# Optimization experiments

Hardware: AMD Instinct MI355X
Metric: run time of the kernel (lower is better)

## Reference

```python
import jax, jax.numpy as jnp
import numpy as np

B, S, H, FMAX, MAXSENT, NHEADS, FFN, SEP = 32, 2048, 768, 32, 64, 12, 3072, 102


def setup_inputs() -> dict:
    key = jax.random.key(0)
    ks = jax.random.split(key, 16)
    sc = 0.02
    ids = jax.random.randint(ks[0], (B, S), 1000, 30000)
    pos = jnp.arange(S)
    # SEP token every 32 positions -> 63 variable-span 'sentences' per row
    ids = jnp.where((pos[None, :] % 32 == 0) & (pos[None, :] > 0), SEP, ids)
    n = lambda k, shp: sc * jax.random.normal(k, shp, jnp.float32)
    return {
        "hidden1": jax.random.normal(ks[1], (B, S, H), jnp.float32),
        "fact_cls": jax.random.normal(ks[2], (B, FMAX, H), jnp.float32),
        "Wp": n(ks[3], (H, H)), "bp": jnp.zeros((H,), jnp.float32), "vp": n(ks[4], (H, 1)),
        "Wq": n(ks[5], (H, H)), "bq": jnp.zeros((H,), jnp.float32),
        "Wk": n(ks[6], (H, H)), "bk": jnp.zeros((H,), jnp.float32),
        "Wv": n(ks[7], (H, H)), "bv": jnp.zeros((H,), jnp.float32),
        "Wo": n(ks[8], (H, H)), "bo": jnp.zeros((H,), jnp.float32),
        "ln1g": jnp.ones((H,), jnp.float32), "ln1b": jnp.zeros((H,), jnp.float32),
        "Wf1": n(ks[9], (H, FFN)), "bf1": jnp.zeros((FFN,), jnp.float32),
        "Wf2": n(ks[10], (FFN, H)), "bf2": jnp.zeros((H,), jnp.float32),
        "ln2g": jnp.ones((H,), jnp.float32), "ln2b": jnp.zeros((H,), jnp.float32),
        "input_ids": ids,
        "facts_count": jax.random.randint(ks[11], (B,), 0, FMAX),
        "max_sent": MAXSENT,
        "sep_id": SEP,
    }


def _ln(x, g, b):
    mu = jnp.mean(x, axis=-1, keepdims=True)
    var = jnp.mean((x - mu) ** 2, axis=-1, keepdims=True)
    return (x - mu) * jax.lax.rsqrt(var + 1e-12) * g + b


def _forward(hidden1, fact_cls, Wp, bp, vp, Wq, bq, Wk, bk, Wv, bv, Wo, bo,
             ln1g, ln1b, Wf1, bf1, Wf2, bf2, ln2g, ln2b,
             input_ids, facts_count, max_sent, sep_id):
    B_, S_ = input_ids.shape
    H_ = hidden1.shape[-1]
    # ---- ragged sentence spans: tokens strictly between SEPs, starting at pos 1 ----
    is_sep = input_ids == sep_id                      # [B,S]
    n_sent = jnp.sum(is_sep, axis=-1)                 # [B]
    seg = jnp.cumsum(is_sep, axis=1) - is_sep         # exclusive cumsum: sentence id per token
    pos = jnp.arange(S_)
    valid = (pos[None, :] >= 1) & (~is_sep) & (seg < n_sent[:, None])
    nseg = B_ * max_sent
    seg_id = jnp.where(valid, jnp.arange(B_)[:, None] * max_sent + seg, nseg).reshape(-1)
    # ---- attention pooling per sentence (segment softmax) ----
    scores = jnp.squeeze(jnp.tanh(hidden1 @ Wp + bp) @ vp, -1).reshape(-1)  # [B*S]
    vflat = valid.reshape(-1)
    m = jax.ops.segment_max(scores, seg_id, num_segments=nseg + 1)
    e = jnp.where(vflat, jnp.exp(scores - m[seg_id]), 0.0)
    z = jax.ops.segment_sum(e, seg_id, num_segments=nseg + 1)
    z = jnp.where(z > 0, z, 1.0)
    w = e / z[seg_id]
    sent = jax.ops.segment_sum(w[:, None] * hidden1.reshape(-1, H_), seg_id,
                               num_segments=nseg + 1)[:nseg].reshape(B_, max_sent, H_)
    # zero-sentence rows fall back to CLS embedding in slot 0
    sent = sent.at[:, 0].set(jnp.where((n_sent == 0)[:, None], hidden1[:, 0], sent[:, 0]))
    n_eff = jnp.maximum(n_sent, 1)
    # ---- pack sentences then facts into dense zero-padded buffer ----
    FMAX_ = fact_cls.shape[1]
    L = max_sent + FMAX_
    bidx = jnp.arange(B_)[:, None]
    buf = jnp.zeros((B_, L + 1, H_), hidden1.dtype)  # extra trash column L
    spos = jnp.where(jnp.arange(max_sent)[None, :] < n_eff[:, None],
                     jnp.arange(max_sent)[None, :], L)
    buf = buf.at[bidx, spos].set(sent)
    fpos = jnp.where(jnp.arange(FMAX_)[None, :] < facts_count[:, None],
                     n_eff[:, None] + jnp.arange(FMAX_)[None, :], L)
    buf = buf.at[bidx, fpos].set(fact_cls)
    x = buf[:, :L]
    amask = (jnp.arange(L)[None, :] < (n_eff + facts_count)[:, None]).astype(x.dtype)
    # ---- tf2 encoder layer (BERT post-LN) on packed sequence ----
    nh = NHEADS
    dh = H_ // nh
    q = (x @ Wq + bq).reshape(B_, L, nh, dh)
    k = (x @ Wk + bk).reshape(B_, L, nh, dh)
    v = (x @ Wv + bv).reshape(B_, L, nh, dh)
    att = jnp.einsum('blhd,bmhd->bhlm', q, k) / np.sqrt(dh).astype(x.dtype)
    att = att + (1.0 - amask)[:, None, None, :] * jnp.asarray(-1e9, x.dtype)
    att = jax.nn.softmax(att, axis=-1)
    ctx = jnp.einsum('bhlm,bmhd->blhd', att, v).reshape(B_, L, H_)
    x = _ln(x + ctx @ Wo + bo, ln1g, ln1b)
    h = jax.nn.gelu(x @ Wf1 + bf1, approximate=False) @ Wf2 + bf2
    x = _ln(x + h, ln2g, ln2b)
    return x[:, 0, :]


def reference(hidden1, fact_cls, Wp, bp, vp, Wq, bq, Wk, bk, Wv, bv, Wo, bo,
              ln1g, ln1b, Wf1, bf1, Wf2, bf2, ln2g, ln2b,
              input_ids, facts_count, max_sent, sep_id):
    return _forward(hidden1, fact_cls, Wp, bp, vp, Wq, bq, Wk, bk, Wv, bv, Wo, bo,
                    ln1g, ln1b, Wf1, bf1, Wf2, bf2, ln2g, ln2b,
                    input_ids, facts_count, max_sent, sep_id)
```

## Files before the change

kernel.cpp:

```cpp
#include <hip/hip_runtime.h>
#include <math.h>

#define Bz   32
#define Sz   2048
#define Hz   768
#define FMAXz 32
#define MSz  64
#define NHz  12
#define DHz  64
#define Lz   96
#define FFNz 3072
#define NTOK (Bz*Sz)

typedef short bf16x8 __attribute__((ext_vector_type(8)));
typedef float f32x4 __attribute__((ext_vector_type(4)));

__device__ __forceinline__ unsigned short f2bf(float f) {
  unsigned u = __float_as_uint(f);
  unsigned r = (u + 0x7fffu + ((u >> 16) & 1u)) >> 16;
  return (unsigned short)r;
}

__device__ __forceinline__ float fast_tanh(float x) {
  float e = __expf(2.0f * x);
  return 1.0f - 2.0f / (e + 1.0f);
}

__device__ __forceinline__ void gload16(const void* gp, void* lp) {
  __builtin_amdgcn_global_load_lds(
      (const __attribute__((address_space(1))) unsigned int*)(unsigned long long)(uintptr_t)gp,
      (__attribute__((address_space(3))) unsigned int*)(unsigned int)(uintptr_t)lp,
      16, 0, 0);
}

__global__ __launch_bounds__(256) void k_seg(
    const int* __restrict__ ids, const int* __restrict__ sep_p,
    int* __restrict__ segid, int* __restrict__ seppos,
    int* __restrict__ nsent, int* __restrict__ neff)
{
  int b = blockIdx.x, tid = threadIdx.x;
  int sep = *sep_p;
  __shared__ int cnt[256];
  __shared__ int total_s;
  const int* row = &ids[b*Sz];
  int base = tid*8;
  int loc[8];
  int c = 0;
  #pragma unroll
  for (int i = 0; i < 8; i++) { loc[i] = row[base+i]; c += (loc[i]==sep) ? 1 : 0; }
  cnt[tid] = c;
  __syncthreads();
  if (tid == 0) {
    int run = 0;
    for (int t = 0; t < 256; t++) { int tmp = cnt[t]; cnt[t] = run; run += tmp; }
    total_s = run;
    nsent[b] = run;
    neff[b]  = run > 0 ? run : 1;
  }
  __syncthreads();
  int total = total_s;
  int seg = cnt[tid];
  #pragma unroll
  for (int i = 0; i < 8; i++) {
    int s = base + i;
    bool issep = (loc[i]==sep);
    if (issep && seg < MSz) seppos[b*MSz + seg] = s;
    bool valid = (s >= 1) && !issep && (seg < total);
    segid[b*Sz + s] = valid ? seg : -1;
    if (issep) seg++;
  }
}

__global__ __launch_bounds__(256) void k_cvt_bf16(
    const float* __restrict__ src, unsigned short* __restrict__ dst, int n4)
{
  int i = blockIdx.x*256 + threadIdx.x;
  if (i >= n4) return;
  float4 v = ((const float4*)src)[i];
  ushort4 o;
  o.x = f2bf(v.x); o.y = f2bf(v.y); o.z = f2bf(v.z); o.w = f2bf(v.w);
  ((ushort4*)dst)[i] = o;
}

__global__ __launch_bounds__(256) void k_tr_cvt(
    const float* __restrict__ src, unsigned short* __restrict__ dst,
    int rows, int cols)
{
  __shared__ float t[32][33];
  int c0 = blockIdx.x*32, r0 = blockIdx.y*32;
  int cx = threadIdx.x & 31, ry = threadIdx.x >> 5;
  #pragma unroll
  for (int p = 0; p < 4; p++)
    t[ry + p*8][cx] = src[(size_t)(r0 + ry + p*8)*cols + c0 + cx];
  __syncthreads();
  #pragma unroll
  for (int p = 0; p < 4; p++) {
    int i = ry + p*8;
    dst[(size_t)(c0 + i)*rows + r0 + cx] = f2bf(t[cx][i]);
  }
}

__global__ __launch_bounds__(256) void k_scores_mfma(
    const unsigned short* __restrict__ h1b, const unsigned short* __restrict__ wpT,
    const float* __restrict__ bp, const float* __restrict__ vp,
    float* __restrict__ scores)
{
  __shared__ unsigned short As[4096];
  __shared__ unsigned short Bs[4096];
  __shared__ float bps[128], vps[128];
  const int tid = threadIdx.x;
  const int wave = tid >> 6, lane = tid & 63;
  const int ml = lane & 15, kg = lane >> 4;
  const int j0 = blockIdx.x * 128;
  const size_t tok0 = (size_t)blockIdx.y * 128;
  if (tid < 128) { bps[tid] = bp[j0+tid]; vps[tid] = vp[j0+tid]; }
  f32x4 acc[2][8];
  #pragma unroll
  for (int rt = 0; rt < 2; rt++)
    #pragma unroll
    for (int ct = 0; ct < 8; ct++) acc[rt][ct] = (f32x4){0.f,0.f,0.f,0.f};
  for (int k0 = 0; k0 < Hz; k0 += 32) {
    __syncthreads();
    #pragma unroll
    for (int l = 0; l < 2; l++) {
      int slot = l*256 + tid;
      int m = slot & 127, kgs = slot >> 7;
      gload16(&h1b[(tok0 + m)*Hz + k0 + kgs*8], &As[slot*8]);
      gload16(&wpT[(size_t)(j0 + m)*Hz + k0 + kgs*8], &Bs[slot*8]);
    }
    __syncthreads();
    bf16x8 af0 = *(const bf16x8*)&As[(kg*128 + wave*32 + ml)*8];
    bf16x8 af1 = *(const bf16x8*)&As[(kg*128 + wave*32 + 16 + ml)*8];
    #pragma unroll
    for (int ct = 0; ct < 8; ct++) {
      bf16x8 bfr = *(const bf16x8*)&Bs[(kg*128 + ct*16 + ml)*8];
      acc[0][ct] = __builtin_amdgcn_mfma_f32_16x16x32_bf16(af0, bfr, acc[0][ct], 0, 0, 0);
      acc[1][ct] = __builtin_amdgcn_mfma_f32_16x16x32_bf16(af1, bfr, acc[1][ct], 0, 0, 0);
    }
  }
  float part[2][4] = {{0,0,0,0},{0,0,0,0}};
  #pragma unroll
  for (int ct = 0; ct < 8; ct++) {
    int cl = ct*16 + ml;
    float bpv = bps[cl], vpv = vps[cl];
    #pragma unroll
    for (int rt = 0; rt < 2; rt++)
      #pragma unroll
      for (int i = 0; i < 4; i++)
        part[rt][i] += fast_tanh(acc[rt][ct][i] + bpv) * vpv;
  }
  #pragma unroll
  for (int rt = 0; rt < 2; rt++)
    #pragma unroll
    for (int i = 0; i < 4; i++) {
      float v = part[rt][i];
      v += __shfl_xor(v, 1); v += __shfl_xor(v, 2);
      v += __shfl_xor(v, 4); v += __shfl_xor(v, 8);
      if (ml == 0) atomicAdd(&scores[tok0 + wave*32 + rt*16 + kg*4 + i], v);
    }
}

__device__ inline unsigned fenc(float f){ unsigned u = __float_as_uint(f); return (u & 0x80000000u) ? ~u : (u | 0x80000000u); }
__device__ inline float fdec(unsigned u){ return (u & 0x80000000u) ? __uint_as_float(u & 0x7fffffffu) : __uint_as_float(~u); }

__global__ __launch_bounds__(256) void k_softmax_seg(
    const float* __restrict__ scores, const int* __restrict__ segid,
    float* __restrict__ w)
{
  int b = blockIdx.x, tid = threadIdx.x;
  __shared__ unsigned menc[MSz];
  __shared__ float msh[MSz];
  __shared__ float zsh[MSz];
  if (tid < MSz) { menc[tid] = 0u; zsh[tid] = 0.f; }
  __syncthreads();
  for (int s = tid; s < Sz; s += 256) {
    int g = segid[b*Sz + s];
    if (g >= 0 && g < MSz) atomicMax(&menc[g], fenc(scores[b*Sz+s]));
  }
  __syncthreads();
  if (tid < MSz) msh[tid] = fdec(menc[tid]);
  __syncthreads();
  for (int s = tid; s < Sz; s += 256) {
    int g = segid[b*Sz + s];
    float e = 0.f;
    if (g >= 0 && g < MSz) { e = expf(scores[b*Sz+s] - msh[g]); atomicAdd(&zsh[g], e); }
    w[b*Sz + s] = e;
  }
  __syncthreads();
  if (tid < MSz) zsh[tid] = (zsh[tid] > 0.f) ? 1.0f/zsh[tid] : 1.0f;
  __syncthreads();
  for (int s = tid; s < Sz; s += 256) {
    int g = segid[b*Sz + s];
    if (g >= 0 && g < MSz) w[b*Sz + s] *= zsh[g];
  }
}

__global__ __launch_bounds__(256) void k_sent(
    const float* __restrict__ h1, const float* __restrict__ w,
    const int* __restrict__ seppos, const int* __restrict__ nsent,
    const int* __restrict__ neff, float* __restrict__ x)
{
  int s = blockIdx.x, b = blockIdx.y, tid = threadIdx.x;
  int ne = neff[b], ns = nsent[b];
  if (s >= ne) return;
  float* xr = &x[((size_t)b*Lz + s)*Hz];
  if (ns == 0) {
    const float* hr = &h1[(size_t)b*Sz*Hz];
    xr[tid] = hr[tid]; xr[tid+256] = hr[tid+256]; xr[tid+512] = hr[tid+512];
    return;
  }
  int start = (s == 0) ? 1 : seppos[b*MSz + s - 1] + 1;
  int end = seppos[b*MSz + s];
  float a0=0.f, a1=0.f, a2=0.f;
  for (int t = start; t < end; t++) {
    float wv = w[b*Sz + t];
    const float* hr = &h1[((size_t)b*Sz + t)*Hz];
    a0 += wv*hr[tid]; a1 += wv*hr[tid+256]; a2 += wv*hr[tid+512];
  }
  xr[tid]=a0; xr[tid+256]=a1; xr[tid+512]=a2;
}

__global__ __launch_bounds__(256) void k_facts(
    const float* __restrict__ fc, const int* __restrict__ fcnt,
    const int* __restrict__ neff, float* __restrict__ x)
{
  int f = blockIdx.x, b = blockIdx.y, tid = threadIdx.x;
  if (f >= fcnt[b]) return;
  int pos = neff[b] + f;
  if (pos >= Lz) return;
  float* xr = &x[((size_t)b*Lz + pos)*Hz];
  const float* fr = &fc[((size_t)b*FMAXz + f)*Hz];
  xr[tid] = fr[tid]; xr[tid+256] = fr[tid+256]; xr[tid+512] = fr[tid+512];
}

__global__ __launch_bounds__(256) void k_packb(
    const float* __restrict__ bk, const float* __restrict__ bv, float* __restrict__ bcat)
{
  int i = blockIdx.x*256 + threadIdx.x;
  if (i < Hz) bcat[i] = bk[i];
  else if (i < 2*Hz) bcat[i] = bv[i - Hz];
}

__global__ __launch_bounds__(256) void k_kv_mfma(
    const unsigned short* __restrict__ xb, const unsigned short* __restrict__ wkvT,
    const float* __restrict__ bcat, float* __restrict__ kv)
{
  __shared__ unsigned short As[4096];
  __shared__ unsigned short Bs[4096];
  const int tid = threadIdx.x;
  const int wave = tid >> 6, lane = tid & 63;
  const int ml = lane & 15, kg = lane >> 4;
  const int j0 = blockIdx.x * 128;
  const size_t m0 = (size_t)blockIdx.y * 128;
  f32x4 acc[2][8];
  #pragma unroll
  for (int rt = 0; rt < 2; rt++)
    #pragma unroll
    for (int ct = 0; ct < 8; ct++) acc[rt][ct] = (f32x4){0.f,0.f,0.f,0.f};
  for (int k0 = 0; k0 < Hz; k0 += 32) {
    __syncthreads();
    #pragma unroll
    for (int l = 0; l < 2; l++) {
      int slot = l*256 + tid;
      int m = slot & 127, kgs = slot >> 7;
      gload16(&xb[(m0 + m)*Hz + k0 + kgs*8], &As[slot*8]);
      gload16(&wkvT[(size_t)(j0 + m)*Hz + k0 + kgs*8], &Bs[slot*8]);
    }
    __syncthreads();
    bf16x8 af0 = *(const bf16x8*)&As[(kg*128 + wave*32 + ml)*8];
    bf16x8 af1 = *(const bf16x8*)&As[(kg*128 + wave*32 + 16 + ml)*8];
    #pragma unroll
    for (int ct = 0; ct < 8; ct++) {
      bf16x8 bfr = *(const bf16x8*)&Bs[(kg*128 + ct*16 + ml)*8];
      acc[0][ct] = __builtin_amdgcn_mfma_f32_16x16x32_bf16(af0, bfr, acc[0][ct], 0, 0, 0);
      acc[1][ct] = __builtin_amdgcn_mfma_f32_16x16x32_bf16(af1, bfr, acc[1][ct], 0, 0, 0);
    }
  }
  #pragma unroll
  for (int ct = 0; ct < 8; ct++) {
    int col = j0 + ct*16 + ml;
    float bb = bcat[col];
    #pragma unroll
    for (int rt = 0; rt < 2; rt++)
      #pragma unroll
      for (int i = 0; i < 4; i++) {
        size_t row = m0 + wave*32 + rt*16 + kg*4 + i;
        kv[row*1536 + col] = acc[rt][ct][i] + bb;
      }
  }
}

__global__ __launch_bounds__(256) void k_gemv_part(
    const float* __restrict__ A, int astr, int aparts, const float* __restrict__ abias,
    int agelu, const float* __restrict__ W, float* __restrict__ part, int N)
{
  __shared__ float As2[32*196];
  __shared__ float red[4][32][64];
  const int tid = threadIdx.x;
  const int k0 = blockIdx.y * 192;
  {
    int b = tid >> 3, t8 = tid & 7;
    #pragma unroll
    for (int i = 0; i < 24; i++) {
      int kk = t8*24 + i;
      float v;
      if (aparts == 0) {
        v = A[(size_t)b*astr + k0 + kk];
      } else {
        v = abias[k0 + kk];
        for (int p = 0; p < aparts; p++) v += A[((size_t)p*32 + b)*astr + k0 + kk];
        if (agelu) v = 0.5f*v*(1.0f + erff(v*0.70710678118654752f));
      }
      As2[b*196 + kk] = v;
    }
  }
  __syncthreads();
  const int jc = tid & 63, w = tid >> 6;
  const int j = blockIdx.x*64 + jc;
  float acc[32];
  #pragma unroll
  for (int b = 0; b < 32; b++) acc[b] = 0.f;
  for (int kq = 0; kq < 12; kq++) {
    int kk = w*48 + kq*4;
    float w0 = W[(size_t)(k0+kk  )*N + j];
    float w1 = W[(size_t)(k0+kk+1)*N + j];
    float w2 = W[(size_t)(k0+kk+2)*N + j];
    float w3 = W[(size_t)(k0+kk+3)*N + j];
    #pragma unroll
    for (int b = 0; b < 32; b++) {
      float4 a = *(const float4*)&As2[b*196 + kk];
      acc[b] += a.x*w0 + a.y*w1 + a.z*w2 + a.w*w3;
    }
  }
  #pragma unroll
  for (int b = 0; b < 32; b++) red[w][b][jc] = acc[b];
  __syncthreads();
  #pragma unroll
  for (int r = 0; r < 8; r++) {
    int o = r*256 + tid;
    int b = o >> 6, jc2 = o & 63;
    float s = red[0][b][jc2] + red[1][b][jc2] + red[2][b][jc2] + red[3][b][jc2];
    part[((size_t)blockIdx.y*32 + b)*N + blockIdx.x*64 + jc2] = s;
  }
}

__global__ __launch_bounds__(128) void k_attn(
    const float* __restrict__ qpart, const float* __restrict__ bq,
    const float* __restrict__ kv,
    const int* __restrict__ neff, const int* __restrict__ fcnt,
    float* __restrict__ ctx0)
{
  int h = blockIdx.x, b = blockIdx.y, tid = threadIdx.x;
  __shared__ float att[Lz];
  __shared__ float qsh[DHz];
  __shared__ float inv_s;
  if (tid < DHz) {
    int col = h*DHz + tid;
    float qv = bq[col];
    #pragma unroll
    for (int p = 0; p < 4; p++) qv += qpart[((size_t)p*32 + b)*Hz + col];
    qsh[tid] = qv;
  }
  __syncthreads();
  int lv = neff[b] + fcnt[b];
  if (tid < Lz) {
    const float* kr = &kv[((size_t)b*Lz + tid)*1536 + h*DHz];
    float s = 0.f;
    #pragma unroll
    for (int d = 0; d < DHz; d++) s += qsh[d]*kr[d];
    s *= 0.125f;
    if (tid >= lv) s -= 1e9f;
    att[tid] = s;
  }
  __syncthreads();
  if (tid == 0) {
    float m = att[0];
    for (int i = 1; i < Lz; i++) m = fmaxf(m, att[i]);
    float z = 0.f;
    for (int i = 0; i < Lz; i++) { float e = expf(att[i] - m); att[i] = e; z += e; }
    inv_s = 1.f/z;
  }
  __syncthreads();
  float inv = inv_s;
  if (tid < DHz) {
    float cvv = 0.f;
    for (int m2 = 0; m2 < Lz; m2++)
      cvv += att[m2] * kv[((size_t)b*Lz + m2)*1536 + Hz + h*DHz + tid];
    ctx0[b*Hz + h*DHz + tid] = cvv*inv;
  }
}

__device__ inline float block_sum_256(float v, float* red)
{
  int tid = threadIdx.x;
  red[tid] = v; __syncthreads();
  for (int off = 128; off > 0; off >>= 1) {
    if (tid < off) red[tid] += red[tid + off];
    __syncthreads();
  }
  float r = red[0];
  __syncthreads();
  return r;
}

__global__ __launch_bounds__(256) void k_ln32_fold(
    const float* __restrict__ part, int P,
    const float* __restrict__ bias,
    const float* __restrict__ resid, int rstr,
    const float* __restrict__ g, const float* __restrict__ bt,
    float* __restrict__ out)
{
  int b = blockIdx.x, tid = threadIdx.x;
  __shared__ float red[256];
  float a0 = bias[tid]     + resid[(size_t)b*rstr + tid];
  float a1 = bias[tid+256] + resid[(size_t)b*rstr + tid+256];
  float a2 = bias[tid+512] + resid[(size_t)b*rstr + tid+512];
  for (int p = 0; p < P; p++) {
    const float* pr = &part[((size_t)p*32 + b)*Hz];
    a0 += pr[tid]; a1 += pr[tid+256]; a2 += pr[tid+512];
  }
  float mu = block_sum_256(a0+a1+a2, red) * (1.0f/Hz);
  float d0=a0-mu, d1=a1-mu, d2=a2-mu;
  float var = block_sum_256(d0*d0+d1*d1+d2*d2, red) * (1.0f/Hz);
  float rs = rsqrtf(var + 1e-12f);
  out[b*Hz+tid]     = d0*rs*g[tid]     + bt[tid];
  out[b*Hz+tid+256] = d1*rs*g[tid+256] + bt[tid+256];
  out[b*Hz+tid+512] = d2*rs*g[tid+512] + bt[tid+512];
}

extern "C" void kernel_launch(void* const* d_in, const int* in_sizes, int n_in,
                              void* d_out, int out_size, void* d_ws, size_t ws_size,
                              hipStream_t stream)
{
  (void)in_sizes; (void)n_in; (void)out_size; (void)ws_size;
  const float* hidden1  = (const float*)d_in[0];
  const float* fact_cls = (const float*)d_in[1];
  const float* Wp   = (const float*)d_in[2];
  const float* bp   = (const float*)d_in[3];
  const float* vp   = (const float*)d_in[4];
  const float* Wq   = (const float*)d_in[5];
  const float* bq   = (const float*)d_in[6];
  const float* Wk   = (const float*)d_in[7];
  const float* bk   = (const float*)d_in[8];
  const float* Wv   = (const float*)d_in[9];
  const float* bv   = (const float*)d_in[10];
  const float* Wo   = (const float*)d_in[11];
  const float* bo   = (const float*)d_in[12];
  const float* ln1g = (const float*)d_in[13];
  const float* ln1b = (const float*)d_in[14];
  const float* Wf1  = (const float*)d_in[15];
  const float* bf1  = (const float*)d_in[16];
  const float* Wf2  = (const float*)d_in[17];
  const float* bf2  = (const float*)d_in[18];
  const float* ln2g = (const float*)d_in[19];
  const float* ln2b = (const float*)d_in[20];
  const int* input_ids   = (const int*)d_in[21];
  const int* facts_count = (const int*)d_in[22];
  const int* sep_id      = (const int*)d_in[24];

  char* ws = (char*)d_ws;
  size_t off = 0;
  auto alloc = [&](size_t bytes) -> void* {
    void* p = ws + off; off += (bytes + 255) & ~(size_t)255; return p;
  };
  unsigned short* h1b  = (unsigned short*)alloc(sizeof(short)*(size_t)NTOK*Hz);
  unsigned short* wpT  = (unsigned short*)alloc(sizeof(short)*(size_t)Hz*Hz);
  unsigned short* wkvT = (unsigned short*)alloc(sizeof(short)*(size_t)Hz*1536);
  unsigned short* xb   = (unsigned short*)alloc(sizeof(short)*(size_t)Bz*Lz*Hz);
  float* x      = (float*)alloc(sizeof(float)*(size_t)Bz*Lz*Hz);
  float* kv     = (float*)alloc(sizeof(float)*(size_t)Bz*Lz*1536);
  float* bcat   = (float*)alloc(sizeof(float)*1536);
  float* scores = (float*)alloc(sizeof(float)*NTOK);
  float* w      = (float*)alloc(sizeof(float)*NTOK);
  int*   segid  = (int*)alloc(sizeof(int)*NTOK);
  int*   seppos = (int*)alloc(sizeof(int)*Bz*MSz);
  int*   nsent  = (int*)alloc(sizeof(int)*Bz);
  int*   neff   = (int*)alloc(sizeof(int)*Bz);
  float* qpart  = (float*)alloc(sizeof(float)*4*Bz*Hz);
  float* ctx0   = (float*)alloc(sizeof(float)*Bz*Hz);
  float* wopart = (float*)alloc(sizeof(float)*4*Bz*Hz);
  float* y0     = (float*)alloc(sizeof(float)*Bz*Hz);
  float* fpart  = (float*)alloc(sizeof(float)*4*Bz*FFNz);
  float* f2part = (float*)alloc(sizeof(float)*16*Bz*Hz);

  k_cvt_bf16<<<(NTOK*Hz/4 + 255)/256, 256, 0, stream>>>(hidden1, h1b, NTOK*Hz/4);
  k_tr_cvt<<<dim3(Hz/32, Hz/32), 256, 0, stream>>>(Wp, wpT, Hz, Hz);
  k_seg<<<Bz, 256, 0, stream>>>(input_ids, sep_id, segid, seppos, nsent, neff);

  hipMemsetAsync(scores, 0, sizeof(float)*NTOK, stream);
  k_scores_mfma<<<dim3(6, NTOK/128), 256, 0, stream>>>(h1b, wpT, bp, vp, scores);
  k_softmax_seg<<<Bz, 256, 0, stream>>>(scores, segid, w);

  hipMemsetAsync(x, 0, sizeof(float)*(size_t)Bz*Lz*Hz, stream);
  k_sent<<<dim3(MSz, Bz), 256, 0, stream>>>(hidden1, w, seppos, nsent, neff, x);
  k_facts<<<dim3(FMAXz, Bz), 256, 0, stream>>>(fact_cls, facts_count, neff, x);
  k_cvt_bf16<<<(Bz*Lz*Hz/4 + 255)/256, 256, 0, stream>>>(x, xb, Bz*Lz*Hz/4);

  k_tr_cvt<<<dim3(Hz/32, Hz/32), 256, 0, stream>>>(Wk, wkvT, Hz, Hz);
  k_tr_cvt<<<dim3(Hz/32, Hz/32), 256, 0, stream>>>(Wv, wkvT + (size_t)Hz*Hz, Hz, Hz);
  k_packb<<<6, 256, 0, stream>>>(bk, bv, bcat);
  k_kv_mfma<<<dim3(12, Bz*Lz/128), 256, 0, stream>>>(xb, wkvT, bcat, kv);

  k_gemv_part<<<dim3(Hz/64, 4), 256, 0, stream>>>(x, Lz*Hz, 0, nullptr, 0, Wq, qpart, Hz);
  k_attn<<<dim3(NHz, Bz), 128, 0, stream>>>(qpart, bq, kv, neff, facts_count, ctx0);
  k_gemv_part<<<dim3(Hz/64, 4), 256, 0, stream>>>(ctx0, Hz, 0, nullptr, 0, Wo, wopart, Hz);
  k_ln32_fold<<<Bz, 256, 0, stream>>>(wopart, 4, bo, x, Lz*Hz, ln1g, ln1b, y0);

  k_gemv_part<<<dim3(FFNz/64, 4), 256, 0, stream>>>(y0, Hz, 0, nullptr, 0, Wf1, fpart, FFNz);
  k_gemv_part<<<dim3(Hz/64, 16), 256, 0, stream>>>(fpart, FFNz, 4, bf1, 1, Wf2, f2part, Hz);
  k_ln32_fold<<<Bz, 256, 0, stream>>>(f2part, 16, bf2, y0, Hz, ln2g, ln2b, (float*)d_out);
}
```

Baseline: 718.3 us.

## Fuse prep kernels, use bf16 hidden in sentence pooling, deepen GEMM K-tiles

Merges the three weight transpose kernels into one launch, and fuses sentence pooling, fact copy and bf16 conversion of x into a single build kernel. Replaces the atomic segmented softmax with a per-sentence wave softmax driven by separator positions, which removes the segid array. Sentence pooling now reads the bf16 copy of hidden1 instead of fp32, which halves that traffic but lowers precision. It also doubles the K tile in the score and KV MFMA GEMMs, shrinks the KV M tile for more blocks, and merges the memsets into one. The aim is to cut launch count and memory traffic.

```diff
diff --git a/kernel.cpp b/kernel.cpp
--- a/kernel.cpp
+++ b/kernel.cpp
@@ -20,12 +20,13 @@
   unsigned r = (u + 0x7fffu + ((u >> 16) & 1u)) >> 16;
   return (unsigned short)r;
 }
-
+__device__ __forceinline__ float bf2f(unsigned short h) {
+  return __uint_as_float(((unsigned)h) << 16);
+}
 __device__ __forceinline__ float fast_tanh(float x) {
   float e = __expf(2.0f * x);
   return 1.0f - 2.0f / (e + 1.0f);
 }
-
 __device__ __forceinline__ void gload16(const void* gp, void* lp) {
   __builtin_amdgcn_global_load_lds(
       (const __attribute__((address_space(1))) unsigned int*)(unsigned long long)(uintptr_t)gp,
@@ -35,13 +36,11 @@
 
 __global__ __launch_bounds__(256) void k_seg(
     const int* __restrict__ ids, const int* __restrict__ sep_p,
-    int* __restrict__ segid, int* __restrict__ seppos,
-    int* __restrict__ nsent, int* __restrict__ neff)
+    int* __restrict__ seppos, int* __restrict__ nsent, int* __restrict__ neff)
 {
   int b = blockIdx.x, tid = threadIdx.x;
   int sep = *sep_p;
   __shared__ int cnt[256];
-  __shared__ int total_s;
   const int* row = &ids[b*Sz];
   int base = tid*8;
   int loc[8];
@@ -53,20 +52,15 @@
   if (tid == 0) {
     int run = 0;
     for (int t = 0; t < 256; t++) { int tmp = cnt[t]; cnt[t] = run; run += tmp; }
-    total_s = run;
     nsent[b] = run;
     neff[b]  = run > 0 ? run : 1;
   }
   __syncthreads();
-  int total = total_s;
   int seg = cnt[tid];
   #pragma unroll
   for (int i = 0; i < 8; i++) {
-    int s = base + i;
     bool issep = (loc[i]==sep);
-    if (issep && seg < MSz) seppos[b*MSz + seg] = s;
-    bool valid = (s >= 1) && !issep && (seg < total);
-    segid[b*Sz + s] = valid ? seg : -1;
+    if (issep && seg < MSz) seppos[b*MSz + seg] = base + i;
     if (issep) seg++;
   }
 }
@@ -82,21 +76,28 @@
   ((ushort4*)dst)[i] = o;
 }
 
-__global__ __launch_bounds__(256) void k_tr_cvt(
-    const float* __restrict__ src, unsigned short* __restrict__ dst,
-    int rows, int cols)
-{
+__global__ __launch_bounds__(256) void k_tr3(
+    const float* __restrict__ Wp, const float* __restrict__ Wk,
+    const float* __restrict__ Wv, unsigned short* __restrict__ wpT,
+    unsigned short* __restrict__ wkvT)
+{
+  int which = blockIdx.x / (Hz/32);
+  int bx = blockIdx.x % (Hz/32);
+  const float* src; unsigned short* dst;
+  if (which == 0)      { src = Wp; dst = wpT; }
+  else if (which == 1) { src = Wk; dst = wkvT; }
+  else                 { src = Wv; dst = wkvT + (size_t)Hz*Hz; }
   __shared__ float t[32][33];
-  int c0 = blockIdx.x*32, r0 = blockIdx.y*32;
+  int c0 = bx*32, r0 = blockIdx.y*32;
   int cx = threadIdx.x & 31, ry = threadIdx.x >> 5;
   #pragma unroll
   for (int p = 0; p < 4; p++)
-    t[ry + p*8][cx] = src[(size_t)(r0 + ry + p*8)*cols + c0 + cx];
+    t[ry + p*8][cx] = src[(size_t)(r0 + ry + p*8)*Hz + c0 + cx];
   __syncthreads();
   #pragma unroll
   for (int p = 0; p < 4; p++) {
     int i = ry + p*8;
-    dst[(size_t)(c0 + i)*rows + r0 + cx] = f2bf(t[cx][i]);
+    dst[(size_t)(c0 + i)*Hz + r0 + cx] = f2bf(t[cx][i]);
   }
 }
 
@@ -105,8 +106,8 @@
     const float* __restrict__ bp, const float* __restrict__ vp,
     float* __restrict__ scores)
 {
-  __shared__ unsigned short As[4096];
-  __shared__ unsigned short Bs[4096];
+  __shared__ unsigned short As[8192];
+  __shared__ unsigned short Bs[8192];
   __shared__ float bps[128], vps[128];
   const int tid = threadIdx.x;
   const int wave = tid >> 6, lane = tid & 63;
@@ -119,23 +120,27 @@
   for (int rt = 0; rt < 2; rt++)
     #pragma unroll
     for (int ct = 0; ct < 8; ct++) acc[rt][ct] = (f32x4){0.f,0.f,0.f,0.f};
-  for (int k0 = 0; k0 < Hz; k0 += 32) {
+  for (int k0 = 0; k0 < Hz; k0 += 64) {
     __syncthreads();
     #pragma unroll
-    for (int l = 0; l < 2; l++) {
+    for (int l = 0; l < 4; l++) {
       int slot = l*256 + tid;
       int m = slot & 127, kgs = slot >> 7;
       gload16(&h1b[(tok0 + m)*Hz + k0 + kgs*8], &As[slot*8]);
       gload16(&wpT[(size_t)(j0 + m)*Hz + k0 + kgs*8], &Bs[slot*8]);
     }
     __syncthreads();
-    bf16x8 af0 = *(const bf16x8*)&As[(kg*128 + wave*32 + ml)*8];
-    bf16x8 af1 = *(const bf16x8*)&As[(kg*128 + wave*32 + 16 + ml)*8];
-    #pragma unroll
-    for (int ct = 0; ct < 8; ct++) {
-      bf16x8 bfr = *(const bf16x8*)&Bs[(kg*128 + ct*16 + ml)*8];
-      acc[0][ct] = __builtin_amdgcn_mfma_f32_16x16x32_bf16(af0, bfr, acc[0][ct], 0, 0, 0);
-      acc[1][ct] = __builtin_amdgcn_mfma_f32_16x16x32_bf16(af1, bfr, acc[1][ct], 0, 0, 0);
+    #pragma unroll
+    for (int s = 0; s < 2; s++) {
+      int kb = s*4 + kg;
+      bf16x8 af0 = *(const bf16x8*)&As[(kb*128 + wave*32 + ml)*8];
+      bf16x8 af1 = *(const bf16x8*)&As[(kb*128 + wave*32 + 16 + ml)*8];
+      #pragma unroll
+      for (int ct = 0; ct < 8; ct++) {
+        bf16x8 bfr = *(const bf16x8*)&Bs[(kb*128 + ct*16 + ml)*8];
+        acc[0][ct] = __builtin_amdgcn_mfma_f32_16x16x32_bf16(af0, bfr, acc[0][ct], 0, 0, 0);
+        acc[1][ct] = __builtin_amdgcn_mfma_f32_16x16x32_bf16(af1, bfr, acc[1][ct], 0, 0, 0);
+      }
     }
   }
   float part[2][4] = {{0,0,0,0},{0,0,0,0}};
@@ -160,133 +165,124 @@
     }
 }
 
-__device__ inline unsigned fenc(float f){ unsigned u = __float_as_uint(f); return (u & 0x80000000u) ? ~u : (u | 0x80000000u); }
-__device__ inline float fdec(unsigned u){ return (u & 0x80000000u) ? __uint_as_float(u & 0x7fffffffu) : __uint_as_float(~u); }
-
-__global__ __launch_bounds__(256) void k_softmax_seg(
-    const float* __restrict__ scores, const int* __restrict__ segid,
-    float* __restrict__ w)
-{
-  int b = blockIdx.x, tid = threadIdx.x;
-  __shared__ unsigned menc[MSz];
-  __shared__ float msh[MSz];
-  __shared__ float zsh[MSz];
-  if (tid < MSz) { menc[tid] = 0u; zsh[tid] = 0.f; }
-  __syncthreads();
-  for (int s = tid; s < Sz; s += 256) {
-    int g = segid[b*Sz + s];
-    if (g >= 0 && g < MSz) atomicMax(&menc[g], fenc(scores[b*Sz+s]));
-  }
-  __syncthreads();
-  if (tid < MSz) msh[tid] = fdec(menc[tid]);
-  __syncthreads();
-  for (int s = tid; s < Sz; s += 256) {
-    int g = segid[b*Sz + s];
-    float e = 0.f;
-    if (g >= 0 && g < MSz) { e = expf(scores[b*Sz+s] - msh[g]); atomicAdd(&zsh[g], e); }
-    w[b*Sz + s] = e;
-  }
-  __syncthreads();
-  if (tid < MSz) zsh[tid] = (zsh[tid] > 0.f) ? 1.0f/zsh[tid] : 1.0f;
-  __syncthreads();
-  for (int s = tid; s < Sz; s += 256) {
-    int g = segid[b*Sz + s];
-    if (g >= 0 && g < MSz) w[b*Sz + s] *= zsh[g];
-  }
-}
-
-__global__ __launch_bounds__(256) void k_sent(
-    const float* __restrict__ h1, const float* __restrict__ w,
+__global__ __launch_bounds__(256) void k_softmax_seg2(
+    const float* __restrict__ scores, const int* __restrict__ seppos,
+    const int* __restrict__ nsent, float* __restrict__ w)
+{
+  int b = blockIdx.x;
+  int wv = threadIdx.x >> 6, lane = threadIdx.x & 63;
+  int ns = nsent[b]; if (ns > MSz) ns = MSz;
+  const float* sc = &scores[b*Sz];
+  float* wr = &w[b*Sz];
+  for (int s = wv; s < ns; s += 4) {
+    int start = (s == 0) ? 1 : seppos[b*MSz + s - 1] + 1;
+    int end = seppos[b*MSz + s];
+    if (end <= start) continue;
+    float m = -1e30f;
+    for (int t = start + lane; t < end; t += 64) m = fmaxf(m, sc[t]);
+    #pragma unroll
+    for (int o = 32; o; o >>= 1) m = fmaxf(m, __shfl_xor(m, o));
+    float z = 0.f;
+    for (int t = start + lane; t < end; t += 64) z += __expf(sc[t] - m);
+    #pragma unroll
+    for (int o = 32; o; o >>= 1) z += __shfl_xor(z, o);
+    float inv = 1.0f / z;
+    for (int t = start + lane; t < end; t += 64) wr[t] = __expf(sc[t] - m) * inv;
+  }
+}
+
+__global__ __launch_bounds__(256) void k_build(
+    const unsigned short* __restrict__ h1b, const float* __restrict__ h1,
+    const float* __restrict__ fc, const float* __restrict__ w,
     const int* __restrict__ seppos, const int* __restrict__ nsent,
-    const int* __restrict__ neff, float* __restrict__ x)
+    const int* __restrict__ neff, const int* __restrict__ fcnt,
+    float* __restrict__ x, unsigned short* __restrict__ xb)
 {
   int s = blockIdx.x, b = blockIdx.y, tid = threadIdx.x;
   int ne = neff[b], ns = nsent[b];
-  if (s >= ne) return;
-  float* xr = &x[((size_t)b*Lz + s)*Hz];
-  if (ns == 0) {
-    const float* hr = &h1[(size_t)b*Sz*Hz];
-    xr[tid] = hr[tid]; xr[tid+256] = hr[tid+256]; xr[tid+512] = hr[tid+512];
-    return;
-  }
-  int start = (s == 0) ? 1 : seppos[b*MSz + s - 1] + 1;
-  int end = seppos[b*MSz + s];
-  float a0=0.f, a1=0.f, a2=0.f;
-  for (int t = start; t < end; t++) {
-    float wv = w[b*Sz + t];
-    const float* hr = &h1[((size_t)b*Sz + t)*Hz];
-    a0 += wv*hr[tid]; a1 += wv*hr[tid+256]; a2 += wv*hr[tid+512];
-  }
-  xr[tid]=a0; xr[tid+256]=a1; xr[tid+512]=a2;
-}
-
-__global__ __launch_bounds__(256) void k_facts(
-    const float* __restrict__ fc, const int* __restrict__ fcnt,
-    const int* __restrict__ neff, float* __restrict__ x)
-{
-  int f = blockIdx.x, b = blockIdx.y, tid = threadIdx.x;
-  if (f >= fcnt[b]) return;
-  int pos = neff[b] + f;
-  if (pos >= Lz) return;
-  float* xr = &x[((size_t)b*Lz + pos)*Hz];
-  const float* fr = &fc[((size_t)b*FMAXz + f)*Hz];
-  xr[tid] = fr[tid]; xr[tid+256] = fr[tid+256]; xr[tid+512] = fr[tid+512];
-}
-
-__global__ __launch_bounds__(256) void k_packb(
-    const float* __restrict__ bk, const float* __restrict__ bv, float* __restrict__ bcat)
-{
-  int i = blockIdx.x*256 + threadIdx.x;
-  if (i < Hz) bcat[i] = bk[i];
-  else if (i < 2*Hz) bcat[i] = bv[i - Hz];
+  float a0, a1, a2;
+  size_t row;
+  if (s < MSz) {
+    if (s >= ne) return;
+    row = (size_t)b*Lz + s;
+    if (ns == 0) {
+      const float* hr = &h1[(size_t)b*Sz*Hz];
+      a0 = hr[tid]; a1 = hr[tid+256]; a2 = hr[tid+512];
+    } else {
+      int start = (s == 0) ? 1 : seppos[b*MSz + s - 1] + 1;
+      int end = seppos[b*MSz + s];
+      a0 = a1 = a2 = 0.f;
+      for (int t = start; t < end; t++) {
+        float wv = w[b*Sz + t];
+        const unsigned short* hr = &h1b[((size_t)b*Sz + t)*Hz];
+        a0 += wv*bf2f(hr[tid]); a1 += wv*bf2f(hr[tid+256]); a2 += wv*bf2f(hr[tid+512]);
+      }
+    }
+  } else {
+    int f = s - MSz;
+    if (f >= fcnt[b]) return;
+    int pos = ne + f;
+    if (pos >= Lz) return;
+    row = (size_t)b*Lz + pos;
+    const float* fr = &fc[((size_t)b*FMAXz + f)*Hz];
+    a0 = fr[tid]; a1 = fr[tid+256]; a2 = fr[tid+512];
+  }
+  float* xr = &x[row*Hz];
+  unsigned short* xbr = &xb[row*Hz];
+  xr[tid] = a0; xr[tid+256] = a1; xr[tid+512] = a2;
+  xbr[tid] = f2bf(a0); xbr[tid+256] = f2bf(a1); xbr[tid+512] = f2bf(a2);
 }
 
 __global__ __launch_bounds__(256) void k_kv_mfma(
     const unsigned short* __restrict__ xb, const unsigned short* __restrict__ wkvT,
-    const float* __restrict__ bcat, float* __restrict__ kv)
+    const float* __restrict__ bk, const float* __restrict__ bv,
+    float* __restrict__ kv)
 {
   __shared__ unsigned short As[4096];
-  __shared__ unsigned short Bs[4096];
+  __shared__ unsigned short Bs[8192];
   const int tid = threadIdx.x;
   const int wave = tid >> 6, lane = tid & 63;
   const int ml = lane & 15, kg = lane >> 4;
   const int j0 = blockIdx.x * 128;
-  const size_t m0 = (size_t)blockIdx.y * 128;
-  f32x4 acc[2][8];
-  #pragma unroll
-  for (int rt = 0; rt < 2; rt++)
-    #pragma unroll
-    for (int ct = 0; ct < 8; ct++) acc[rt][ct] = (f32x4){0.f,0.f,0.f,0.f};
-  for (int k0 = 0; k0 < Hz; k0 += 32) {
+  const size_t m0 = (size_t)blockIdx.y * 64;
+  f32x4 acc[8];
+  #pragma unroll
+  for (int ct = 0; ct < 8; ct++) acc[ct] = (f32x4){0.f,0.f,0.f,0.f};
+  for (int k0 = 0; k0 < Hz; k0 += 64) {
     __syncthreads();
     #pragma unroll
     for (int l = 0; l < 2; l++) {
       int slot = l*256 + tid;
+      int m = slot & 63, kgs = slot >> 6;
+      gload16(&xb[(m0 + m)*Hz + k0 + kgs*8], &As[slot*8]);
+    }
+    #pragma unroll
+    for (int l = 0; l < 4; l++) {
+      int slot = l*256 + tid;
       int m = slot & 127, kgs = slot >> 7;
-      gload16(&xb[(m0 + m)*Hz + k0 + kgs*8], &As[slot*8]);
       gload16(&wkvT[(size_t)(j0 + m)*Hz + k0 + kgs*8], &Bs[slot*8]);
     }
     __syncthreads();
-    bf16x8 af0 = *(const bf16x8*)&As[(kg*128 + wave*32 + ml)*8];
-    bf16x8 af1 = *(const bf16x8*)&As[(kg*128 + wave*32 + 16 + ml)*8];
-    #pragma unroll
-    for (int ct = 0; ct < 8; ct++) {
-      bf16x8 bfr = *(const bf16x8*)&Bs[(kg*128 + ct*16 + ml)*8];
-      acc[0][ct] = __builtin_amdgcn_mfma_f32_16x16x32_bf16(af0, bfr, acc[0][ct], 0, 0, 0);
-      acc[1][ct] = __builtin_amdgcn_mfma_f32_16x16x32_bf16(af1, bfr, acc[1][ct], 0, 0, 0);
+    #pragma unroll
+    for (int s = 0; s < 2; s++) {
+      int kb = s*4 + kg;
+      bf16x8 af = *(const bf16x8*)&As[(kb*64 + wave*16 + ml)*8];
+      #pragma unroll
+      for (int ct = 0; ct < 8; ct++) {
+        bf16x8 bfr = *(const bf16x8*)&Bs[(kb*128 + ct*16 + ml)*8];
+        acc[ct] = __builtin_amdgcn_mfma_f32_16x16x32_bf16(af, bfr, acc[ct], 0, 0, 0);
+      }
     }
   }
   #pragma unroll
   for (int ct = 0; ct < 8; ct++) {
     int col = j0 + ct*16 + ml;
-    float bb = bcat[col];
-    #pragma unroll
-    for (int rt = 0; rt < 2; rt++)
-      #pragma unroll
-      for (int i = 0; i < 4; i++) {
-        size_t row = m0 + wave*32 + rt*16 + kg*4 + i;
-        kv[row*1536 + col] = acc[rt][ct][i] + bb;
-      }
+    float bb = (col < Hz) ? bk[col] : bv[col - Hz];
+    #pragma unroll
+    for (int i = 0; i < 4; i++) {
+      size_t row = m0 + wave*16 + kg*4 + i;
+      kv[row*1536 + col] = acc[ct][i] + bb;
+    }
   }
 }
 
@@ -377,7 +373,7 @@
     float m = att[0];
     for (int i = 1; i < Lz; i++) m = fmaxf(m, att[i]);
     float z = 0.f;
-    for (int i = 0; i < Lz; i++) { float e = expf(att[i] - m); att[i] = e; z += e; }
+    for (int i = 0; i < Lz; i++) { float e = __expf(att[i] - m); att[i] = e; z += e; }
     inv_s = 1.f/z;
   }
   __syncthreads();
@@ -463,16 +459,16 @@
   auto alloc = [&](size_t bytes) -> void* {
     void* p = ws + off; off += (bytes + 255) & ~(size_t)255; return p;
   };
+  float* scores        = (float*)alloc(sizeof(float)*NTOK);
+  unsigned short* xb   = (unsigned short*)alloc(sizeof(short)*(size_t)Bz*Lz*Hz);
+  float* x             = (float*)alloc(sizeof(float)*(size_t)Bz*Lz*Hz);
+  size_t zbytes = (char*)(x + (size_t)Bz*Lz*Hz) - (char*)scores;
+
   unsigned short* h1b  = (unsigned short*)alloc(sizeof(short)*(size_t)NTOK*Hz);
   unsigned short* wpT  = (unsigned short*)alloc(sizeof(short)*(size_t)Hz*Hz);
   unsigned short* wkvT = (unsigned short*)alloc(sizeof(short)*(size_t)Hz*1536);
-  unsigned short* xb   = (unsigned short*)alloc(sizeof(short)*(size_t)Bz*Lz*Hz);
-  float* x      = (float*)alloc(sizeof(float)*(size_t)Bz*Lz*Hz);
   float* kv     = (float*)alloc(sizeof(float)*(size_t)Bz*Lz*1536);
-  float* bcat   = (float*)alloc(sizeof(float)*1536);
-  float* scores = (float*)alloc(sizeof(float)*NTOK);
   float* w      = (float*)alloc(sizeof(float)*NTOK);
-  int*   segid  = (int*)alloc(sizeof(int)*NTOK);
   int*   seppos = (int*)alloc(sizeof(int)*Bz*MSz);
   int*   nsent  = (int*)alloc(sizeof(int)*Bz);
   int*   neff   = (int*)alloc(sizeof(int)*Bz);
@@ -483,23 +479,18 @@
   float* fpart  = (float*)alloc(sizeof(float)*4*Bz*FFNz);
   float* f2part = (float*)alloc(sizeof(float)*16*Bz*Hz);
 
+  hipMemsetAsync(scores, 0, zbytes, stream);
   k_cvt_bf16<<<(NTOK*Hz/4 + 255)/256, 256, 0, stream>>>(hidden1, h1b, NTOK*Hz/4);
-  k_tr_cvt<<<dim3(Hz/32, Hz/32), 256, 0, stream>>>(Wp, wpT, Hz, Hz);
-  k_seg<<<Bz, 256, 0, stream>>>(input_ids, sep_id, segid, seppos, nsent, neff);
-
-  hipMemsetAsync(scores, 0, sizeof(float)*NTOK, stream);
+  k_tr3<<<dim3(3*(Hz/32), Hz/32), 256, 0, stream>>>(Wp, Wk, Wv, wpT, wkvT);
+  k_seg<<<Bz, 256, 0, stream>>>(input_ids, sep_id, seppos, nsent, neff);
+
   k_scores_mfma<<<dim3(6, NTOK/128), 256, 0, stream>>>(h1b, wpT, bp, vp, scores);
-  k_softmax_seg<<<Bz, 256, 0, stream>>>(scores, segid, w);
-
-  hipMemsetAsync(x, 0, sizeof(float)*(size_t)Bz*Lz*Hz, stream);
-  k_sent<<<dim3(MSz, Bz), 256, 0, stream>>>(hidden1, w, seppos, nsent, neff, x);
-  k_facts<<<dim3(FMAXz, Bz), 256, 0, stream>>>(fact_cls, facts_count, neff, x);
-  k_cvt_bf16<<<(Bz*Lz*Hz/4 + 255)/256, 256, 0, stream>>>(x, xb, Bz*Lz*Hz/4);
-
-  k_tr_cvt<<<dim3(Hz/32, Hz/32), 256, 0, stream>>>(Wk, wkvT, Hz, Hz);
-  k_tr_cvt<<<dim3(Hz/32, Hz/32), 256, 0, stream>>>(Wv, wkvT + (size_t)Hz*Hz, Hz, Hz);
-  k_packb<<<6, 256, 0, stream>>>(bk, bv, bcat);
-  k_kv_mfma<<<dim3(12, Bz*Lz/128), 256, 0, stream>>>(xb, wkvT, bcat, kv);
+  k_softmax_seg2<<<Bz, 256, 0, stream>>>(scores, seppos, nsent, w);
+
+  k_build<<<dim3(MSz + FMAXz, Bz), 256, 0, stream>>>(
+      h1b, hidden1, fact_cls, w, seppos, nsent, neff, facts_count, x, xb);
+
+  k_kv_mfma<<<dim3(12, Bz*Lz/64), 256, 0, stream>>>(xb, wkvT, bk, bv, kv);
 
   k_gemv_part<<<dim3(Hz/64, 4), 256, 0, stream>>>(x, Lz*Hz, 0, nullptr, 0, Wq, qpart, Hz);
   k_attn<<<dim3(NHz, Bz), 128, 0, stream>>>(qpart, bq, kv, neff, facts_count, ctx0);
```

Measured after the change: 716.3 us. About the same (-0.3%).
